# Performance work log

Hardware: AMD Instinct MI355X
Metric: run time of the kernel (lower is better)

Reference implementation:

```python
import jax, jax.numpy as jnp
import numpy as np

LORA_RANK = 16
LORA_ALPHA = 32
CHUNK_SIZE = 256
TTT_LR = 0.01
CLIP_THRESHOLD = 1.0
SCALING = LORA_ALPHA / LORA_RANK
LN_EPS = 1e-5


def setup_inputs() -> dict:
    key = jax.random.key(0)
    ks = jax.random.split(key, 5)
    B, S, K, H = 2, 8192, 1024, 1024
    x = jax.random.normal(ks[0], (B, S, K), dtype=jnp.float32)
    Wb = jax.random.normal(ks[1], (H, K), dtype=jnp.float32) / np.sqrt(K)
    init_A = jax.random.normal(ks[2], (H, LORA_RANK), dtype=jnp.float32) * 0.01
    init_B = jax.random.normal(ks[3], (LORA_RANK, K), dtype=jnp.float32) * 0.01
    ln_gamma = jnp.ones((K,), dtype=jnp.float32)
    ln_beta = jnp.zeros((K,), dtype=jnp.float32)
    Wp = jax.random.normal(ks[4], (H, K), dtype=jnp.float32) / np.sqrt(K)
    return {"x": x, "Wb": Wb, "init_A": init_A, "init_B": init_B,
            "ln_gamma": ln_gamma, "ln_beta": ln_beta, "Wp": Wp}


def _forward(x, Wb, init_A, init_B, ln_gamma, ln_beta, Wp):
    B_sz, Seq, k_dim = x.shape
    h_dim = Wb.shape[0]
    r = init_A.shape[1]
    nc = Seq // CHUNK_SIZE  # Seq chosen divisible; pad_len == 0

    base_out = x @ Wb.T  # [B, S, H]

    # --- target construction under no_grad: LayerNorm + left-shift ---
    xd = jax.lax.stop_gradient(x)
    mu = jnp.mean(xd, axis=-1, keepdims=True)
    var = jnp.mean((xd - mu) ** 2, axis=-1, keepdims=True)
    xn = (xd - mu) * jax.lax.rsqrt(var + LN_EPS) * ln_gamma + ln_beta
    shifted = jnp.pad(xn[:, 1:, :], ((0, 0), (0, 1), (0, 0)))
    shifted = jax.lax.stop_gradient(shifted)

    V = shifted @ Wp.T  # [B, S, H]

    Z = x.reshape(B_sz * nc, CHUNK_SIZE, k_dim)
    Vc = V.reshape(B_sz * nc, CHUNK_SIZE, h_dim)

    # per-chunk fast-weight deltas
    proj_in = Z @ init_B.T                                # [BC, C, r]
    dA = jnp.einsum('bch,bcr->bhr', Vc, proj_in)          # [BC, H, r]
    proj_err = Vc @ init_A                                # [BC, C, r]
    dB = jnp.einsum('bcr,bck->brk', proj_err, Z)          # [BC, r, K]

    dA = dA.reshape(B_sz, nc, h_dim, r)
    dB = dB.reshape(B_sz, nc, r, k_dim)

    # exclusive cross-chunk cumsum
    accA = jnp.cumsum(dA, axis=1)
    accB = jnp.cumsum(dB, axis=1)
    accA = jnp.concatenate([jnp.zeros_like(accA[:, :1]), accA[:, :-1]], axis=1)
    accB = jnp.concatenate([jnp.zeros_like(accB[:, :1]), accB[:, :-1]], axis=1)

    lr = TTT_LR * SCALING
    rawA = (lr * accA).reshape(-1, h_dim, r)
    rawB = (lr * accB).reshape(-1, r, k_dim)

    # joint norm clip (norm_type=2)
    norm_sq = (jnp.sum(rawA.astype(jnp.float32) ** 2, axis=(-2, -1), keepdims=True)
               + jnp.sum(rawB.astype(jnp.float32) ** 2, axis=(-2, -1), keepdims=True))
    total_norm = jnp.sqrt(norm_sq)
    coef = jnp.minimum(CLIP_THRESHOLD / (total_norm + 1e-6), 1.0).astype(rawA.dtype)

    A_eff = init_A[None] - rawA * coef  # [BC, H, r]
    B_eff = init_B[None] - rawB * coef  # [BC, r, K]

    mid = jnp.einsum('bck,brk->bcr', Z, B_eff)          # [BC, C, r]
    lora = jnp.einsum('bcr,bhr->bch', mid, A_eff)       # [BC, C, H]
    lora = lora.reshape(B_sz, Seq, h_dim)

    return base_out + lora * SCALING


def reference(x, Wb, init_A, init_B, ln_gamma, ln_beta, Wp):
    return _forward(x, Wb, init_A, init_B, ln_gamma, ln_beta, Wp)
```

## Files before the change

kernel.cpp:

```cpp
#include <hip/hip_runtime.h>

typedef __attribute__((ext_vector_type(8))) short s16x8;
typedef __attribute__((ext_vector_type(4))) float f32x4;
typedef __attribute__((ext_vector_type(2))) float f32x2;
typedef unsigned short u16;

#define B_SZ 2
#define SEQ 8192
#define KD 1024
#define HD 1024
#define RK 16
#define CH 256
#define NCH 64
static constexpr float LR_SC = 0.02f;
static constexpr float SCALE_OUT = 2.0f;

__device__ __forceinline__ u16 f2b(float f) {
  union { float f; unsigned int u; } c; c.f = f;
  unsigned int u = c.u;
  unsigned int r = (u + 0x7fffu + ((u >> 16) & 1u)) >> 16;
  return (u16)r;
}
__device__ __forceinline__ float b2f(u16 v) {
  union { unsigned int u; float f; } c; c.u = ((unsigned int)v) << 16; return c.f;
}
__device__ __forceinline__ void async16(const u16* g, u16* l) {
  __builtin_amdgcn_global_load_lds((const __attribute__((address_space(1))) void*)g,
                                   (__attribute__((address_space(3))) void*)l, 16, 0, 0);
}

__global__ __launch_bounds__(256) void cvt_all(const float* __restrict__ Wb,
                                               const float* __restrict__ Wp,
                                               const float* __restrict__ initB,
                                               u16* __restrict__ Wbb,
                                               u16* __restrict__ Wpb,
                                               u16* __restrict__ iBb) {
  int bid = blockIdx.x;
  const float* src; u16* dst; int base;
  if (bid < 1024)      { src = Wb;    dst = Wbb; base = bid; }
  else if (bid < 2048) { src = Wp;    dst = Wpb; base = bid - 1024; }
  else                 { src = initB; dst = iBb; base = bid - 2048; }
  int i = (base * 256 + threadIdx.x) * 4;
  float4 v = *(const float4*)(src + i);
  ushort4 o; o.x = f2b(v.x); o.y = f2b(v.y); o.z = f2b(v.z); o.w = f2b(v.w);
  *(ushort4*)(dst + i) = o;
}

__global__ __launch_bounds__(256) void wpat_part(const float* __restrict__ initA,
                                                 const float* __restrict__ Wp,
                                                 float* __restrict__ part) {
  int t = threadIdx.x;
  int k = blockIdx.x * 256 + t;
  int hseg = blockIdx.y;
  __shared__ float Asm[64 * 16];
  *(float4*)&Asm[t * 4] = *(const float4*)&initA[(size_t)hseg * 1024 + t * 4];
  __syncthreads();
  float acc[16];
  #pragma unroll
  for (int j = 0; j < 16; j++) acc[j] = 0.f;
  const float* wp = Wp + (size_t)hseg * 64 * KD + k;
  #pragma unroll 8
  for (int hh = 0; hh < 64; hh++) {
    float w = wp[(size_t)hh * KD];
    const float4* ar = (const float4*)&Asm[hh * 16];
    #pragma unroll
    for (int qq = 0; qq < 4; qq++) {
      float4 a = ar[qq];
      acc[qq*4+0] += w * a.x; acc[qq*4+1] += w * a.y;
      acc[qq*4+2] += w * a.z; acc[qq*4+3] += w * a.w;
    }
  }
  float* o = part + ((size_t)hseg * 1024 + k) * 16;
  #pragma unroll
  for (int qq = 0; qq < 4; qq++) {
    float4 r; r.x = acc[qq*4]; r.y = acc[qq*4+1]; r.z = acc[qq*4+2]; r.w = acc[qq*4+3];
    *(float4*)&o[qq * 4] = r;
  }
}

__global__ __launch_bounds__(256) void wpat_reduce(const float* __restrict__ part,
                                                   u16* __restrict__ WpAT) {
  int idx = blockIdx.x * 256 + threadIdx.x;
  int k = idx & 1023, r = idx >> 10;
  float s = 0.f;
  #pragma unroll
  for (int seg = 0; seg < 16; seg++)
    s += part[((size_t)seg * 1024 + k) * 16 + r];
  WpAT[(size_t)r * KD + k] = f2b(s);
}

__global__ __launch_bounds__(256) void ln_shift(const float* __restrict__ x,
                                                const float* __restrict__ gamma,
                                                const float* __restrict__ beta,
                                                u16* __restrict__ xb,
                                                u16* __restrict__ shb) {
  int row = blockIdx.x;
  int t = threadIdx.x;
  int s = row & (SEQ - 1);
  const float* xr = x + (size_t)row * KD;
  float4 v = *(const float4*)(xr + t * 4);
  ushort4 o; o.x = f2b(v.x); o.y = f2b(v.y); o.z = f2b(v.z); o.w = f2b(v.w);
  *(ushort4*)(xb + (size_t)row * KD + t * 4) = o;

  if (s == 0) {
    ushort4 z; z.x = 0; z.y = 0; z.z = 0; z.w = 0;
    *(ushort4*)(shb + ((size_t)row + SEQ - 1) * KD + t * 4) = z;
    return;
  }
  float s1 = v.x + v.y + v.z + v.w;
  float s2 = v.x * v.x + v.y * v.y + v.z * v.z + v.w * v.w;
  #pragma unroll
  for (int off = 32; off > 0; off >>= 1) {
    s1 += __shfl_down(s1, off);
    s2 += __shfl_down(s2, off);
  }
  __shared__ float red[8];
  int wave = t >> 6, lane = t & 63;
  if (lane == 0) { red[wave * 2] = s1; red[wave * 2 + 1] = s2; }
  __syncthreads();
  float sum = red[0] + red[2] + red[4] + red[6];
  float ssq = red[1] + red[3] + red[5] + red[7];
  float mu = sum * (1.0f / KD);
  float var = ssq * (1.0f / KD) - mu * mu;
  float rstd = rsqrtf(var + 1e-5f);
  float4 g = *(const float4*)(gamma + t * 4);
  float4 bb = *(const float4*)(beta + t * 4);
  ushort4 so;
  so.x = f2b((v.x - mu) * rstd * g.x + bb.x);
  so.y = f2b((v.y - mu) * rstd * g.y + bb.y);
  so.z = f2b((v.z - mu) * rstd * g.z + bb.z);
  so.w = f2b((v.w - mu) * rstd * g.w + bb.w);
  *(ushort4*)(shb + (size_t)(row - 1) * KD + t * 4) = so;
}

__global__ __launch_bounds__(256, 2) void gemm_fused(const u16* __restrict__ A,
                                                     const u16* __restrict__ Bm,
                                                     const u16* __restrict__ mid2,
                                                     const u16* __restrict__ Aef,
                                                     float* __restrict__ C) {
  constexpr int BM = 128, BN = 128, BK = 64, N = HD, Kd = KD;
  __shared__ u16 As[BM * BK];
  __shared__ u16 Bs[BN * BK];
  int tid = threadIdx.x;
  int lane = tid & 63, wave = tid >> 6;
  int lb = blockIdx.x + 8 * blockIdx.y;
  int q = lb & 7, t = lb >> 3;
  int mb = q * 16 + (t >> 3);
  int nb = t & 7;
  int m0 = mb * 128, n0 = nb * 128;
  int wm = (wave >> 1) * 64, wn = (wave & 1) * 64;
  int lr = lane & 15;
  int qd = lane >> 4;
  int sw = lr & 7;
  int slot0 = ((qd ^ sw) * 8);
  int slot1 = (((4 + qd) ^ sw) * 8);
  f32x4 acc[4][4] = {};

  const u16* gbase; u16* lbase;
  if (wave < 2) { gbase = A + (size_t)(m0 + wave * 64) * Kd; lbase = As + wave * 64 * BK; }
  else          { gbase = Bm + (size_t)(n0 + (wave - 2) * 64) * Kd; lbase = Bs + (wave - 2) * 64 * BK; }
  int srow = lane >> 3;
  int scol = ((lane & 7) ^ srow) * 8;
  const u16* gsrc = gbase + (size_t)srow * Kd + scol;

  for (int k0 = 0; k0 < Kd; k0 += BK) {
    #pragma unroll
    for (int i = 0; i < 8; i++)
      async16(gsrc + (size_t)i * 8 * Kd, lbase + i * 512);
    gsrc += BK;
    __syncthreads();
    s16x8 af[4], bfr[4];
    #pragma unroll
    for (int i = 0; i < 4; i++) af[i] = *(const s16x8*)(As + (wm + i * 16 + lr) * BK + slot0);
    #pragma unroll
    for (int j = 0; j < 4; j++) bfr[j] = *(const s16x8*)(Bs + (wn + j * 16 + lr) * BK + slot0);
    #pragma unroll
    for (int i = 0; i < 4; i++)
      #pragma unroll
      for (int j = 0; j < 4; j++)
        acc[i][j] = __builtin_amdgcn_mfma_f32_16x16x32_bf16(af[i], bfr[j], acc[i][j], 0, 0, 0);
    #pragma unroll
    for (int i = 0; i < 4; i++) af[i] = *(const s16x8*)(As + (wm + i * 16 + lr) * BK + slot1);
    #pragma unroll
    for (int j = 0; j < 4; j++) bfr[j] = *(const s16x8*)(Bs + (wn + j * 16 + lr) * BK + slot1);
    #pragma unroll
    for (int i = 0; i < 4; i++)
      #pragma unroll
      for (int j = 0; j < 4; j++)
        acc[i][j] = __builtin_amdgcn_mfma_f32_16x16x32_bf16(af[i], bfr[j], acc[i][j], 0, 0, 0);
    __syncthreads();
  }

  {
    int chunk = m0 >> 8;
    const u16* abase = Aef + (size_t)chunk * (HD * RK);
    int klane = lane >> 4;
    s16x8 am2[4], bn2[4];
    #pragma unroll
    for (int i = 0; i < 4; i++) {
      if (klane < 2)
        am2[i] = *(const s16x8*)(mid2 + (size_t)(m0 + wm + i * 16 + lr) * RK + klane * 8);
      else { s16x8 z = {}; am2[i] = z; }
    }
    #pragma unroll
    for (int j = 0; j < 4; j++) {
      if (klane < 2)
        bn2[j] = *(const s16x8*)(abase + (size_t)(n0 + wn + j * 16 + lr) * RK + klane * 8);
      else { s16x8 z = {}; bn2[j] = z; }
    }
    #pragma unroll
    for (int i = 0; i < 4; i++)
      #pragma unroll
      for (int j = 0; j < 4; j++)
        acc[i][j] = __builtin_amdgcn_mfma_f32_16x16x32_bf16(am2[i], bn2[j], acc[i][j], 0, 0, 0);
  }

  int rb = (lane >> 4) * 4, cc = lane & 15;
  #pragma unroll
  for (int i = 0; i < 4; i++)
    #pragma unroll
    for (int j = 0; j < 4; j++)
      #pragma unroll
      for (int p = 0; p < 4; p++)
        C[(size_t)(m0 + wm + i * 16 + rb + p) * N + (n0 + wn + j * 16 + cc)] = acc[i][j][p];
}

__global__ __launch_bounds__(256) void rank16_proj(const u16* __restrict__ xb,
                                                   const u16* __restrict__ shb,
                                                   const u16* __restrict__ iBb,
                                                   const u16* __restrict__ WpAT,
                                                   float* __restrict__ pin,
                                                   float* __restrict__ per) {
  const u16* X; const u16* W; float* O;
  if (blockIdx.z == 0) { X = xb; W = iBb; O = pin; }
  else                 { X = shb; W = WpAT; O = per; }
  int wave = threadIdx.x >> 6, lane = threadIdx.x & 63;
  int m0 = (blockIdx.x * 4 + wave) * 16;
  int lr = lane & 15, lk = (lane >> 4) * 8;
  const u16* xp = X + (size_t)(m0 + lr) * KD + lk;
  const u16* wp = W + (size_t)lr * KD + lk;
  f32x4 acc = {};
  #pragma unroll 8
  for (int k0 = 0; k0 < KD; k0 += 32) {
    s16x8 a = *(const s16x8*)xp;
    s16x8 b = *(const s16x8*)wp;
    acc = __builtin_amdgcn_mfma_f32_16x16x32_bf16(a, b, acc, 0, 0, 0);
    xp += 32; wp += 32;
  }
  int rb = (lane >> 4) * 4, cc = lane & 15;
  #pragma unroll
  for (int p = 0; p < 4; p++)
    O[(size_t)(m0 + rb + p) * RK + cc] = acc[p];
}

__global__ __launch_bounds__(256) void rank16_mid(const u16* __restrict__ xb,
                                                  const u16* __restrict__ Bef,
                                                  u16* __restrict__ mid2) {
  int wave = threadIdx.x >> 6, lane = threadIdx.x & 63;
  int m0 = (blockIdx.x * 4 + wave) * 16;
  int chunk = m0 >> 8;
  int lr = lane & 15, lk = (lane >> 4) * 8;
  const u16* xp = xb + (size_t)(m0 + lr) * KD + lk;
  const u16* wp = Bef + (size_t)chunk * (RK * KD) + (size_t)lr * KD + lk;
  f32x4 acc = {};
  #pragma unroll 8
  for (int k0 = 0; k0 < KD; k0 += 32) {
    s16x8 a = *(const s16x8*)xp;
    s16x8 b = *(const s16x8*)wp;
    acc = __builtin_amdgcn_mfma_f32_16x16x32_bf16(a, b, acc, 0, 0, 0);
    xp += 32; wp += 32;
  }
  int rb = (lane >> 4) * 4, cc = lane & 15;
  #pragma unroll
  for (int p = 0; p < 4; p++)
    mid2[(size_t)(m0 + rb + p) * RK + cc] = f2b(SCALE_OUT * acc[p]);
}

__global__ __launch_bounds__(256) void gk_kernel(const u16* __restrict__ xb,
                                                 const u16* __restrict__ shb,
                                                 const float* __restrict__ pin,
                                                 const float* __restrict__ per,
                                                 float* __restrict__ G,
                                                 float* __restrict__ dB) {
  int tile = blockIdx.x;
  int chunk = blockIdx.y;
  int which = blockIdx.z;
  int t = threadIdx.x;
  __shared__ float P[CH * RK];
  const float* psrc = which ? per : pin;
  for (int i = t; i < 1024; i += 256)
    *(float4*)&P[i * 4] = *(const float4*)&psrc[(size_t)chunk * 4096 + i * 4];
  __syncthreads();
  f32x2 acc[8];
  #pragma unroll
  for (int j = 0; j < 8; j++) acc[j] = (f32x2){0.f, 0.f};
  int col = tile * 256 + t;
  const u16* src = (which ? xb : shb) + (size_t)chunk * CH * KD + col;
  #pragma unroll 4
  for (int c = 0; c < 256; c++) {
    float v = b2f(src[(size_t)c * 1024]);
    f32x2 vv = {v, v};
    const f32x2* pr = (const f32x2*)&P[c * 16];
    #pragma unroll
    for (int qq = 0; qq < 8; qq++)
      acc[qq] += vv * pr[qq];
  }
  float* o = (which ? dB : G) + (size_t)chunk * 16384 + col;
  #pragma unroll
  for (int j = 0; j < 8; j++) {
    o[(size_t)(2 * j) * 1024] = acc[j][0];
    o[(size_t)(2 * j + 1) * 1024] = acc[j][1];
  }
}

__global__ __launch_bounds__(256) void cumsum_kernel(const float* __restrict__ G,
                                                     const float* __restrict__ dB,
                                                     u16* __restrict__ rawG,
                                                     float* __restrict__ rawB) {
  int idx = blockIdx.x * 256 + threadIdx.x;
  int which = idx >> 15;
  int rem = idx & 32767;
  int b = rem >> 14;
  int e = rem & 16383;
  size_t base = (size_t)b * 32 * 16384 + e;
  if (which == 0) {
    float run = 0.f;
    for (int i = 0; i < 32; i++) {
      size_t off = base + (size_t)i * 16384;
      float nv = G[off];
      rawG[off] = f2b(LR_SC * run);
      run += nv;
    }
  } else {
    float run = 0.f;
    for (int i = 0; i < 32; i++) {
      size_t off = base + (size_t)i * 16384;
      float nv = dB[off];
      rawB[off] = LR_SC * run;
      run += nv;
    }
  }
}

__global__ __launch_bounds__(256) void dagemm(const u16* __restrict__ Wpb,
                                              const u16* __restrict__ rawG,
                                              float* __restrict__ rawA) {
  int wave = threadIdx.x >> 6, lane = threadIdx.x & 63;
  int m0 = (blockIdx.x * 4 + wave) * 16;
  int chunk = blockIdx.y;
  int lr = lane & 15, lk = (lane >> 4) * 8;
  const u16* ap = Wpb + (size_t)(m0 + lr) * KD + lk;
  const u16* bp = rawG + (size_t)chunk * 16384 + (size_t)lr * KD + lk;
  f32x4 acc = {};
  #pragma unroll 8
  for (int k0 = 0; k0 < KD; k0 += 32) {
    s16x8 a = *(const s16x8*)ap;
    s16x8 b = *(const s16x8*)bp;
    acc = __builtin_amdgcn_mfma_f32_16x16x32_bf16(a, b, acc, 0, 0, 0);
    ap += 32; bp += 32;
  }
  int rb = (lane >> 4) * 4, cc = lane & 15;
  #pragma unroll
  for (int p = 0; p < 4; p++)
    rawA[(size_t)chunk * 16384 + (size_t)(m0 + rb + p) * RK + cc] = acc[p];
}

__global__ __launch_bounds__(1024) void coef_eff(const float* __restrict__ initA,
                                                 const float* __restrict__ initB,
                                                 const float* __restrict__ rawA,
                                                 const float* __restrict__ rawB,
                                                 u16* __restrict__ Aef,
                                                 u16* __restrict__ Bef) {
  int chunk = blockIdx.x, t = threadIdx.x;
  const float* a = rawA + (size_t)chunk * 16384;
  const float* b = rawB + (size_t)chunk * 16384;
  float s = 0.f;
  #pragma unroll
  for (int i = t * 4; i < 16384; i += 4096) {
    float4 v = *(const float4*)(a + i);
    s += v.x*v.x + v.y*v.y + v.z*v.z + v.w*v.w;
    float4 w = *(const float4*)(b + i);
    s += w.x*w.x + w.y*w.y + w.z*w.z + w.w*w.w;
  }
  #pragma unroll
  for (int off = 32; off > 0; off >>= 1) s += __shfl_down(s, off);
  __shared__ float red[16];
  int wave = t >> 6, lane = t & 63;
  if (lane == 0) red[wave] = s;
  __syncthreads();
  float tot = 0.f;
  #pragma unroll
  for (int w = 0; w < 16; w++) tot += red[w];
  float cf = fminf(1.0f / (sqrtf(tot) + 1e-6f), 1.0f);
  u16* ao = Aef + (size_t)chunk * 16384;
  u16* bo = Bef + (size_t)chunk * 16384;
  #pragma unroll
  for (int i = t * 4; i < 16384; i += 4096) {
    float4 iv = *(const float4*)(initA + i);
    float4 rv = *(const float4*)(a + i);
    ushort4 r;
    r.x = f2b(iv.x - rv.x * cf); r.y = f2b(iv.y - rv.y * cf);
    r.z = f2b(iv.z - rv.z * cf); r.w = f2b(iv.w - rv.w * cf);
    *(ushort4*)(ao + i) = r;
    float4 iw = *(const float4*)(initB + i);
    float4 rw = *(const float4*)(b + i);
    ushort4 rr;
    rr.x = f2b(iw.x - rw.x * cf); rr.y = f2b(iw.y - rw.y * cf);
    rr.z = f2b(iw.z - rw.z * cf); rr.w = f2b(iw.w - rw.w * cf);
    *(ushort4*)(bo + i) = rr;
  }
}

extern "C" void kernel_launch(void* const* d_in, const int* in_sizes, int n_in,
                              void* d_out, int out_size, void* d_ws, size_t ws_size,
                              hipStream_t stream) {
  (void)in_sizes; (void)n_in; (void)out_size; (void)ws_size;
  const float* x     = (const float*)d_in[0];
  const float* Wb    = (const float*)d_in[1];
  const float* initA = (const float*)d_in[2];
  const float* initB = (const float*)d_in[3];
  const float* gamma = (const float*)d_in[4];
  const float* beta  = (const float*)d_in[5];
  const float* Wp    = (const float*)d_in[6];
  float* out = (float*)d_out;

  char* ws = (char*)d_ws;
  size_t off = 0;
  auto alloc = [&](size_t bytes) -> void* {
    void* p = ws + off;
    off = (off + bytes + 255) & ~(size_t)255;
    return p;
  };
  const size_t ROWS = (size_t)B_SZ * SEQ;
  u16* xb    = (u16*)alloc(ROWS * KD * 2);
  u16* shb   = (u16*)alloc(ROWS * KD * 2);
  u16* Wbb   = (u16*)alloc((size_t)HD * KD * 2);
  u16* Wpb   = (u16*)alloc((size_t)HD * KD * 2);
  u16* iBb   = (u16*)alloc((size_t)RK * KD * 2);
  u16* WpAT  = (u16*)alloc((size_t)RK * KD * 2);
  float* wpart = (float*)alloc((size_t)16 * KD * RK * 4);
  float* pin = (float*)alloc((size_t)NCH * CH * RK * 4);
  float* per = (float*)alloc((size_t)NCH * CH * RK * 4);
  float* G   = (float*)alloc((size_t)NCH * 16384 * 4);
  float* dB  = (float*)alloc((size_t)NCH * 16384 * 4);
  u16* rawG  = (u16*)alloc((size_t)NCH * 16384 * 2);
  float* rawB= (float*)alloc((size_t)NCH * 16384 * 4);
  float* rawA= (float*)alloc((size_t)NCH * 16384 * 4);
  u16* Aef   = (u16*)alloc((size_t)NCH * 16384 * 2);
  u16* Bef   = (u16*)alloc((size_t)NCH * 16384 * 2);
  u16* mid2  = (u16*)alloc(ROWS * RK * 2);

  cvt_all<<<2064, 256, 0, stream>>>(Wb, Wp, initB, Wbb, Wpb, iBb);
  wpat_part<<<dim3(4, 16), 256, 0, stream>>>(initA, Wp, wpart);
  wpat_reduce<<<64, 256, 0, stream>>>(wpart, WpAT);
  ln_shift<<<ROWS, 256, 0, stream>>>(x, gamma, beta, xb, shb);
  rank16_proj<<<dim3(256, 1, 2), 256, 0, stream>>>(xb, shb, iBb, WpAT, pin, per);
  gk_kernel<<<dim3(4, NCH, 2), 256, 0, stream>>>(xb, shb, pin, per, G, dB);
  cumsum_kernel<<<256, 256, 0, stream>>>(G, dB, rawG, rawB);
  dagemm<<<dim3(16, NCH), 256, 0, stream>>>(Wpb, rawG, rawA);
  coef_eff<<<NCH, 1024, 0, stream>>>(initA, initB, rawA, rawB, Aef, Bef);
  rank16_mid<<<256, 256, 0, stream>>>(xb, Bef, mid2);
  gemm_fused<<<dim3(8, 128), 256, 0, stream>>>(xb, Wbb, mid2, Aef, out);
}
```

Baseline: 281.5 us.

## Stage GEMM epilogue through LDS, split clip-norm kernel, unroll cumsum

The main GEMM epilogue now writes accumulators into an LDS tile (padded rows of 132 floats, reusing the operand buffers) in two halves, then emits coalesced float4 global stores instead of scattered scalar stores. The single 64-block coef_eff kernel becomes two kernels: a 256-block partial norm reduction and a 512-block emit pass, to raise parallelism. The cumsum loops get unroll 8 pragmas. The shared buffer grows to about 33 KB and the epilogue adds barriers, which could affect occupancy at 2 blocks per SM.

New measurement: 285.4 us. No clear change (+1.4%).

```diff
diff --git a/kernel.cpp b/kernel.cpp
--- a/kernel.cpp
+++ b/kernel.cpp
@@ -139,8 +139,10 @@
                                                      const u16* __restrict__ Aef,
                                                      float* __restrict__ C) {
   constexpr int BM = 128, BN = 128, BK = 64, N = HD, Kd = KD;
-  __shared__ u16 As[BM * BK];
-  __shared__ u16 Bs[BN * BK];
+  __shared__ __align__(16) char SMEMRAW[64 * 132 * 4];
+  u16* As = (u16*)SMEMRAW;
+  u16* Bs = (u16*)(SMEMRAW + BM * BK * 2);
+  float* SM = (float*)SMEMRAW;
   int tid = threadIdx.x;
   int lane = tid & 63, wave = tid >> 6;
   int lb = blockIdx.x + 8 * blockIdx.y;
@@ -215,14 +217,32 @@
         acc[i][j] = __builtin_amdgcn_mfma_f32_16x16x32_bf16(am2[i], bn2[j], acc[i][j], 0, 0, 0);
   }
 
-  int rb = (lane >> 4) * 4, cc = lane & 15;
-  #pragma unroll
-  for (int i = 0; i < 4; i++)
-    #pragma unroll
-    for (int j = 0; j < 4; j++)
+  int rb = qd * 4, cc = lr;
+  int row8 = tid >> 3;
+  int fidx = tid & 7;
+  #pragma unroll
+  for (int h = 0; h < 2; h++) {
+    __syncthreads();
+    if ((wave >> 1) == h) {
       #pragma unroll
-      for (int p = 0; p < 4; p++)
-        C[(size_t)(m0 + wm + i * 16 + rb + p) * N + (n0 + wn + j * 16 + cc)] = acc[i][j][p];
+      for (int i = 0; i < 4; i++)
+        #pragma unroll
+        for (int j = 0; j < 4; j++)
+          #pragma unroll
+          for (int p = 0; p < 4; p++)
+            SM[(i * 16 + rb + p) * 132 + wn + j * 16 + cc] = acc[i][j][p];
+    }
+    __syncthreads();
+    #pragma unroll
+    for (int s = 0; s < 2; s++) {
+      int rl = s * 32 + row8;
+      const float* src = SM + rl * 132 + fidx * 4;
+      float* dst = C + (size_t)(m0 + h * 64 + rl) * N + n0 + fidx * 4;
+      #pragma unroll
+      for (int qq = 0; qq < 4; qq++)
+        *(float4*)(dst + qq * 32) = *(const float4*)(src + qq * 32);
+    }
+  }
 }
 
 __global__ __launch_bounds__(256) void rank16_proj(const u16* __restrict__ xb,
@@ -325,6 +345,7 @@
   size_t base = (size_t)b * 32 * 16384 + e;
   if (which == 0) {
     float run = 0.f;
+    #pragma unroll 8
     for (int i = 0; i < 32; i++) {
       size_t off = base + (size_t)i * 16384;
       float nv = G[off];
@@ -333,6 +354,7 @@
     }
   } else {
     float run = 0.f;
+    #pragma unroll 8
     for (int i = 0; i < 32; i++) {
       size_t off = base + (size_t)i * 16384;
       float nv = dB[off];
@@ -365,49 +387,60 @@
     rawA[(size_t)chunk * 16384 + (size_t)(m0 + rb + p) * RK + cc] = acc[p];
 }
 
-__global__ __launch_bounds__(1024) void coef_eff(const float* __restrict__ initA,
+__global__ __launch_bounds__(256) void coef_norm(const float* __restrict__ rawA,
+                                                 const float* __restrict__ rawB,
+                                                 float* __restrict__ part) {
+  int b = blockIdx.x;
+  int chunk = b >> 2, quarter = b & 3;
+  size_t base = (size_t)chunk * 16384 + quarter * 4096;
+  const float* a = rawA + base;
+  const float* bb = rawB + base;
+  int t = threadIdx.x;
+  float s = 0.f;
+  #pragma unroll
+  for (int i = 0; i < 4; i++) {
+    float4 v = *(const float4*)(a + (i * 256 + t) * 4);
+    s += v.x*v.x + v.y*v.y + v.z*v.z + v.w*v.w;
+    float4 w = *(const float4*)(bb + (i * 256 + t) * 4);
+    s += w.x*w.x + w.y*w.y + w.z*w.z + w.w*w.w;
+  }
+  #pragma unroll
+  for (int off = 32; off > 0; off >>= 1) s += __shfl_down(s, off);
+  __shared__ float red[4];
+  int wave = t >> 6, lane = t & 63;
+  if (lane == 0) red[wave] = s;
+  __syncthreads();
+  if (t == 0) part[b] = red[0] + red[1] + red[2] + red[3];
+}
+
+__global__ __launch_bounds__(256) void coef_emit(const float* __restrict__ initA,
                                                  const float* __restrict__ initB,
                                                  const float* __restrict__ rawA,
                                                  const float* __restrict__ rawB,
+                                                 const float* __restrict__ part,
                                                  u16* __restrict__ Aef,
                                                  u16* __restrict__ Bef) {
-  int chunk = blockIdx.x, t = threadIdx.x;
-  const float* a = rawA + (size_t)chunk * 16384;
-  const float* b = rawB + (size_t)chunk * 16384;
-  float s = 0.f;
-  #pragma unroll
-  for (int i = t * 4; i < 16384; i += 4096) {
-    float4 v = *(const float4*)(a + i);
-    s += v.x*v.x + v.y*v.y + v.z*v.z + v.w*v.w;
-    float4 w = *(const float4*)(b + i);
-    s += w.x*w.x + w.y*w.y + w.z*w.z + w.w*w.w;
-  }
-  #pragma unroll
-  for (int off = 32; off > 0; off >>= 1) s += __shfl_down(s, off);
-  __shared__ float red[16];
-  int wave = t >> 6, lane = t & 63;
-  if (lane == 0) red[wave] = s;
-  __syncthreads();
-  float tot = 0.f;
-  #pragma unroll
-  for (int w = 0; w < 16; w++) tot += red[w];
+  int b = blockIdx.x;
+  int chunk = b >> 3, eighth = b & 7;
+  float tot = part[chunk * 4] + part[chunk * 4 + 1] + part[chunk * 4 + 2] + part[chunk * 4 + 3];
   float cf = fminf(1.0f / (sqrtf(tot) + 1e-6f), 1.0f);
-  u16* ao = Aef + (size_t)chunk * 16384;
-  u16* bo = Bef + (size_t)chunk * 16384;
-  #pragma unroll
-  for (int i = t * 4; i < 16384; i += 4096) {
-    float4 iv = *(const float4*)(initA + i);
-    float4 rv = *(const float4*)(a + i);
+  size_t cbase = (size_t)chunk * 16384;
+  int t = threadIdx.x;
+  #pragma unroll
+  for (int i = 0; i < 2; i++) {
+    int idx = eighth * 2048 + (i * 256 + t) * 4;
+    float4 iv = *(const float4*)(initA + idx);
+    float4 rv = *(const float4*)(rawA + cbase + idx);
     ushort4 r;
     r.x = f2b(iv.x - rv.x * cf); r.y = f2b(iv.y - rv.y * cf);
     r.z = f2b(iv.z - rv.z * cf); r.w = f2b(iv.w - rv.w * cf);
-    *(ushort4*)(ao + i) = r;
-    float4 iw = *(const float4*)(initB + i);
-    float4 rw = *(const float4*)(b + i);
+    *(ushort4*)(Aef + cbase + idx) = r;
+    float4 iw = *(const float4*)(initB + idx);
+    float4 rw = *(const float4*)(rawB + cbase + idx);
     ushort4 rr;
     rr.x = f2b(iw.x - rw.x * cf); rr.y = f2b(iw.y - rw.y * cf);
     rr.z = f2b(iw.z - rw.z * cf); rr.w = f2b(iw.w - rw.w * cf);
-    *(ushort4*)(bo + i) = rr;
+    *(ushort4*)(Bef + cbase + idx) = rr;
   }
 }
 
@@ -449,6 +482,7 @@
   u16* Aef   = (u16*)alloc((size_t)NCH * 16384 * 2);
   u16* Bef   = (u16*)alloc((size_t)NCH * 16384 * 2);
   u16* mid2  = (u16*)alloc(ROWS * RK * 2);
+  float* npart = (float*)alloc((size_t)256 * 4);
 
   cvt_all<<<2064, 256, 0, stream>>>(Wb, Wp, initB, Wbb, Wpb, iBb);
   wpat_part<<<dim3(4, 16), 256, 0, stream>>>(initA, Wp, wpart);
@@ -458,7 +492,8 @@
   gk_kernel<<<dim3(4, NCH, 2), 256, 0, stream>>>(xb, shb, pin, per, G, dB);
   cumsum_kernel<<<256, 256, 0, stream>>>(G, dB, rawG, rawB);
   dagemm<<<dim3(16, NCH), 256, 0, stream>>>(Wpb, rawG, rawA);
-  coef_eff<<<NCH, 1024, 0, stream>>>(initA, initB, rawA, rawB, Aef, Bef);
+  coef_norm<<<256, 256, 0, stream>>>(rawA, rawB, npart);
+  coef_emit<<<512, 256, 0, stream>>>(initA, initB, rawA, rawB, npart, Aef, Bef);
   rank16_mid<<<256, 256, 0, stream>>>(xb, Bef, mid2);
   gemm_fused<<<dim3(8, 128), 256, 0, stream>>>(xb, Wbb, mid2, Aef, out);
 }
```
